# Performance work log

Hardware: AMD Instinct MI355X
Metric: run time of the kernel (lower is better)

## Reference

```python
import jax, jax.numpy as jnp
from jax import lax
import numpy as np

B, T = 256, 512
CHAR_SIZE, CHAR_DIM, HIDDEN = 10000, 50, 256
HALF = HIDDEN // 2  # per-direction hidden size


def _lstm_dir(x, Wih, Whh, bih, bhh, reverse):
    # x: [B,T,D]; Wih: [4H,D]; Whh: [4H,H]; gate order i,f,g,o (PyTorch)
    Bsz = x.shape[0]
    H = Whh.shape[1]
    xg = jnp.einsum('btd,gd->btg', x, Wih) + bih + bhh  # precompute input gates [B,T,4H]
    def step(carry, gt):
        h, c = carry
        g = gt + h @ Whh.T
        i, f, gg, o = jnp.split(g, 4, axis=-1)
        c = jax.nn.sigmoid(f) * c + jax.nn.sigmoid(i) * jnp.tanh(gg)
        h = jax.nn.sigmoid(o) * jnp.tanh(c)
        return (h, c), h
    init = (jnp.zeros((Bsz, H), x.dtype), jnp.zeros((Bsz, H), x.dtype))
    _, hs = lax.scan(step, init, jnp.swapaxes(xg, 0, 1), reverse=reverse)
    return jnp.swapaxes(hs, 0, 1)  # [B,T,H]


def setup_inputs() -> dict:
    key = jax.random.key(0)
    ks = jax.random.split(key, 10)
    scale = np.sqrt(3.0 / CHAR_DIM)
    inp = {
        'user_text_idx': jax.random.randint(ks[0], (B, T), 0, CHAR_SIZE),
        'masks': jnp.ones((B, T), jnp.float32),
        'emb': jax.random.uniform(ks[1], (CHAR_SIZE, CHAR_DIM), jnp.float32, -scale, scale),
        'Wih_f': jax.random.normal(ks[2], (4 * HALF, CHAR_DIM), jnp.float32) * 0.08,
        'Whh_f': jax.random.normal(ks[3], (4 * HALF, HALF), jnp.float32) * 0.08,
        'bih_f': jnp.zeros((4 * HALF,), jnp.float32),
        'bhh_f': jnp.zeros((4 * HALF,), jnp.float32),
        'Wih_b': jax.random.normal(ks[4], (4 * HALF, CHAR_DIM), jnp.float32) * 0.08,
        'Whh_b': jax.random.normal(ks[5], (4 * HALF, HALF), jnp.float32) * 0.08,
        'bih_b': jnp.zeros((4 * HALF,), jnp.float32),
        'bhh_b': jnp.zeros((4 * HALF,), jnp.float32),
    }
    return inp


def reference(user_text_idx, masks, emb, Wih_f, Whh_f, bih_f, bhh_f, Wih_b, Whh_b, bih_b, bhh_b):
    x = emb[user_text_idx]                                  # [B,T,D] embedding lookup
    h_f = _lstm_dir(x, Wih_f, Whh_f, bih_f, bhh_f, False)   # forward direction
    h_b = _lstm_dir(x, Wih_b, Whh_b, bih_b, bhh_b, True)    # backward direction
    out = jnp.concatenate([h_f, h_b], axis=-1)              # [B,T,HIDDEN]
    out = out - (1.0 - masks[..., None]) * 1e8              # mask pad positions
    return jnp.max(out, axis=-2)                            # masked max-pool -> [B,HIDDEN]
```

## Files before the change

kernel.cpp:

```cpp
#include <hip/hip_runtime.h>
#include <hip/hip_fp16.h>


#define TT 512
#define CH 2

typedef _Float16 f16;
typedef _Float16 f16x8 __attribute__((ext_vector_type(8)));
typedef float f32x4 __attribute__((ext_vector_type(4)));
typedef unsigned int u32;
typedef unsigned short u16;

static __device__ __forceinline__ u32 packh2(float lo, float hi) {
    union { struct { f16 x, y; } h; u32 u; } cv;
    cv.h.x = (f16)lo; cv.h.y = (f16)hi;
    return cv.u;
}
static __device__ __forceinline__ u16 f16bits(float v) {
    union { f16 h; u16 u; } cv; cv.h = (f16)v; return cv.u;
}
static __device__ __forceinline__ float fexp(float x) {
    return __builtin_amdgcn_exp2f(x * 1.44269504088896341f);
}
static __device__ __forceinline__ float frcp(float x) {
    return __builtin_amdgcn_rcpf(x);
}
static __device__ __forceinline__ float sigf(float x) {
    return frcp(1.f + fexp(-x));
}
static __device__ __forceinline__ float xor8(float x) {
    union { float f; int i; } c; c.f = x;
#if __has_builtin(__builtin_amdgcn_mov_dpp)
    c.i = __builtin_amdgcn_mov_dpp(c.i, 0x128, 0xF, 0xF, 0);
#elif __has_builtin(__builtin_amdgcn_update_dpp)
    c.i = __builtin_amdgcn_update_dpp(c.i, c.i, 0x128, 0xF, 0xF, 0);
#else
    c.i = __builtin_amdgcn_ds_swizzle(c.i, 0x201F);
#endif
    return c.f;
}
static __device__ __forceinline__ float sel4(f32x4 v, int q) {
    return (q & 2) ? ((q & 1) ? v[3] : v[2]) : ((q & 1) ? v[1] : v[0]);
}

__global__ __attribute__((amdgpu_flat_work_group_size(512, 512),
                          amdgpu_waves_per_eu(2, 2)))
void bilstm_mfma_dpp_kernel(const int* __restrict__ idx,
                            const float* __restrict__ masks,
                            const float* __restrict__ emb,
                            const float* __restrict__ Wih_f, const float* __restrict__ Whh_f,
                            const float* __restrict__ bih_f, const float* __restrict__ bhh_f,
                            const float* __restrict__ Wih_b, const float* __restrict__ Whh_b,
                            const float* __restrict__ bih_b, const float* __restrict__ bhh_b,
                            float* __restrict__ out)
{
    __shared__ __align__(16) unsigned char Hbuf[2][6 * 1024];
    __shared__ u16 idx16[CH * TT];
    __shared__ u32 mbits[TT];

    const int tid  = threadIdx.x;
    const int lane = tid & 63;
    const int wv   = tid >> 6;
    const int l15  = lane & 15;
    const int c4   = lane >> 4;
    const int d    = blockIdx.x & 1;
    const int g    = blockIdx.x >> 1;
    const int b0   = g * CH;
    const int rev  = d;

    const int chain = l15 & 1;
    const int cp    = l15 >> 1;
    const int flag  = cp >> 2;
    const int q     = cp & 3;

    const float* Wih = d ? Wih_b : Wih_f;
    const float* Whh = d ? Whh_b : Whh_f;
    const float* bih = d ? bih_b : bih_f;
    const float* bhh = d ? bhh_b : bhh_f;

    for (int i = tid; i < CH * TT; i += 512) {
        const int m = i >> 9, t = i & 511;
        idx16[i] = (u16)idx[(b0 + m) * TT + t];
    }
    if (tid < TT) {
        u32 mb = 0;
        for (int m = 0; m < CH; ++m)
            mb |= (masks[(b0 + m) * TT + tid] != 0.f ? 1u : 0u) << m;
        mbits[tid] = mb;
    }
    for (int i = tid; i < 2 * 6 * 1024 / 4; i += 512)
        ((u32*)Hbuf)[i] = 0u;

    f16x8 w[6][4];
    f32x4 bias4[4];
#pragma unroll
    for (int gt = 0; gt < 4; ++gt) {
        const int n = (wv + gt * 8) * 16 + l15;
        {
            const int nb_ = (wv + gt * 8) * 16 + c4 * 4;
            const float4 bi = *(const float4*)(bih + nb_);
            const float4 bh = *(const float4*)(bhh + nb_);
            bias4[gt][0] = bi.x + bh.x; bias4[gt][1] = bi.y + bh.y;
            bias4[gt][2] = bi.z + bh.z; bias4[gt][3] = bi.w + bh.w;
        }
#pragma unroll
        for (int jj = 0; jj < 4; ++jj) {
            const float2 e = *(const float2*)(Wih + n * 50 + c4 * 8 + jj * 2);
            w[0][gt][2 * jj]     = (f16)e.x;
            w[0][gt][2 * jj + 1] = (f16)e.y;
        }
#pragma unroll
        for (int j = 0; j < 8; ++j) {
            const int k = 32 + c4 * 8 + j;
            float v = 0.f;
            if (k < 50) v = Wih[n * 50 + k];
            w[1][gt][j] = (f16)v;
        }
#pragma unroll
        for (int kt = 2; kt < 6; ++kt) {
            const int kh = (kt - 2) * 32 + c4 * 8;
            const float4 e0 = *(const float4*)(Whh + n * 128 + kh);
            const float4 e1 = *(const float4*)(Whh + n * 128 + kh + 4);
            w[kt][gt][0] = (f16)e0.x; w[kt][gt][1] = (f16)e0.y;
            w[kt][gt][2] = (f16)e0.z; w[kt][gt][3] = (f16)e0.w;
            w[kt][gt][4] = (f16)e1.x; w[kt][gt][5] = (f16)e1.y;
            w[kt][gt][6] = (f16)e1.z; w[kt][gt][7] = (f16)e1.w;
        }
    }

    __syncthreads();

    if (tid < 400) {
        const int pm = tid / 25, ps = tid % 25;
        const int t0  = rev ? (TT - 1) : 0;
        const int row = idx16[(pm & 1) * TT + t0];
        const float2 e = *(const float2*)(emb + row * 50 + ps * 2);
        const int k0 = 2 * ps;
        const int kt = k0 >> 5, c4k = (k0 >> 3) & 3, j = k0 & 7;
        *(u32*)(&Hbuf[0][(kt << 10) + ((c4k * 16 + pm) << 4) + (j << 1)]) =
            packh2(e.x, e.y);
    }
    __syncthreads();

    float cst0 = 0.f, rm0 = -3e38f;

    const int hd     = wv * 16 + c4 * 4 + q;
    const int k0h    = 64 + hd;
    const int wb_kt  = k0h >> 5;
    const int wb_c4k = (k0h >> 3) & 3;
    const int wb_j   = k0h & 7;
    const int wb_off = (wb_kt << 10) + ((wb_c4k * 16 + chain) << 4) + (wb_j << 1)
                     + flag * 128;

    for (int s = 0; s < TT; ++s) {
        const int cur = s & 1;
        const int t   = rev ? (TT - 1 - s) : s;

        float2 e;
        int pk0 = 0;
        const bool pf = (tid < 400) && (s + 1 < TT);
        const int pm = tid / 25, ps = tid % 25;
        if (pf) {
            const int t1  = rev ? (TT - 2 - s) : (s + 1);
            const int row = idx16[(pm & 1) * TT + t1];
            e = *(const float2*)(emb + row * 50 + ps * 2);
            pk0 = 2 * ps;
        }

        const unsigned char* hb = &Hbuf[cur][0];
        f32x4 ai = bias4[0], af = bias4[1], ag = bias4[2], ao = bias4[3];
#pragma unroll
        for (int kt = 0; kt < 6; ++kt) {
            const f16x8 bf = *(const f16x8*)(hb + (kt << 10) + (lane << 4));
            ai = __builtin_amdgcn_mfma_f32_16x16x32_f16(w[kt][0], bf, ai, 0, 0, 0);
            af = __builtin_amdgcn_mfma_f32_16x16x32_f16(w[kt][1], bf, af, 0, 0, 0);
            ag = __builtin_amdgcn_mfma_f32_16x16x32_f16(w[kt][2], bf, ag, 0, 0, 0);
            ao = __builtin_amdgcn_mfma_f32_16x16x32_f16(w[kt][3], bf, ao, 0, 0, 0);
        }

        const float iv = sel4(ai, q);
        const float fv = sel4(af, q);
        const float gv = sel4(ag, q);
        const float ov = sel4(ao, q);

        const bool fB = (flag != 0);
        const float u = fB ? (gv + gv) : fv;
        const float v = fB ? ov : iv;
        const float su = sigf(u);
        const float sv = sigf(v);
        const float tg_send = 2.f * su - 1.f;
        const float tgx = xor8(tg_send);
        const float svx = xor8(sv);
        const float cc = su * cst0 + sv * tgx;
        cst0 = cc;
        const float ccx = xor8(cc);
        const float cc_use = fB ? ccx : cc;
        const float th = 2.f * sigf(cc_use + cc_use) - 1.f;
        const float so_use = fB ? sv : svx;
        const float hh = so_use * th;

        const float pen = ((mbits[t] >> chain) & 1u) ? 0.f : 1e8f;
        rm0 = fmaxf(rm0, hh - pen);

        unsigned char* nb = &Hbuf[cur ^ 1][0];
        {
            const u16 pk = f16bits(hh);
            *(u16*)(nb + wb_off)      = pk;
            *(u16*)(nb + wb_off + 32) = pk;
            *(u16*)(nb + wb_off + 64) = pk;
            *(u16*)(nb + wb_off + 96) = pk;
        }
        if (pf) {
            const int kt = pk0 >> 5, c4k = (pk0 >> 3) & 3, j = pk0 & 7;
            *(u32*)(nb + (kt << 10) + ((c4k * 16 + pm) << 4) + (j << 1)) =
                packh2(e.x, e.y);
        }
        __syncthreads();
    }

    if (!flag) {
        out[(b0 + chain) * 256 + d * 128 + hd] = rm0;
    }
}

extern "C" void kernel_launch(void* const* d_in, const int* in_sizes, int n_in,
                              void* d_out, int out_size, void* d_ws, size_t ws_size,
                              hipStream_t stream) {
    const int*   idx   = (const int*)d_in[0];
    const float* masks = (const float*)d_in[1];
    const float* emb   = (const float*)d_in[2];
    const float* Wih_f = (const float*)d_in[3];
    const float* Whh_f = (const float*)d_in[4];
    const float* bih_f = (const float*)d_in[5];
    const float* bhh_f = (const float*)d_in[6];
    const float* Wih_b = (const float*)d_in[7];
    const float* Whh_b = (const float*)d_in[8];
    const float* bih_b = (const float*)d_in[9];
    const float* bhh_b = (const float*)d_in[10];
    float* out = (float*)d_out;

    bilstm_mfma_dpp_kernel<<<dim3(256), dim3(512), 0, stream>>>(
        idx, masks, emb,
        Wih_f, Whh_f, bih_f, bhh_f,
        Wih_b, Whh_b, bih_b, bhh_b,
        out);
}
```

Measured before the change: 397.8 us.

## Compact LDS hidden-state buffer and cut per-step shared stores

Replaces the 12 KB pre-swizzled MFMA B-operand buffer with a compact per-chain [2][CH][192] f16 vector. Each lane now reads its B fragment with a broadcast-style 16-byte load, so the layout no longer duplicates rows. Hidden writes go from four u16 stores per lane to one packed u32 store from a quarter of the lanes, using a DPP lane exchange to pair neighbours. Embedding prefetch moves to 50 threads in the last wave. The aim is to shrink LDS write traffic and bank conflicts on the per-step critical path, at the cost of an extra DPP op and a possible read-side broadcast pattern.

```diff
diff --git a/kernel.cpp b/kernel.cpp
--- a/kernel.cpp
+++ b/kernel.cpp
@@ -16,9 +16,6 @@
     cv.h.x = (f16)lo; cv.h.y = (f16)hi;
     return cv.u;
 }
-static __device__ __forceinline__ u16 f16bits(float v) {
-    union { f16 h; u16 u; } cv; cv.h = (f16)v; return cv.u;
-}
 static __device__ __forceinline__ float fexp(float x) {
     return __builtin_amdgcn_exp2f(x * 1.44269504088896341f);
 }
@@ -30,13 +27,12 @@
 }
 static __device__ __forceinline__ float xor8(float x) {
     union { float f; int i; } c; c.f = x;
-#if __has_builtin(__builtin_amdgcn_mov_dpp)
-    c.i = __builtin_amdgcn_mov_dpp(c.i, 0x128, 0xF, 0xF, 0);
-#elif __has_builtin(__builtin_amdgcn_update_dpp)
-    c.i = __builtin_amdgcn_update_dpp(c.i, c.i, 0x128, 0xF, 0xF, 0);
-#else
-    c.i = __builtin_amdgcn_ds_swizzle(c.i, 0x201F);
-#endif
+    c.i = __builtin_amdgcn_mov_dpp(c.i, 0x128, 0xF, 0xF, false);
+    return c.f;
+}
+static __device__ __forceinline__ float xor2(float x) {
+    union { float f; int i; } c; c.f = x;
+    c.i = __builtin_amdgcn_mov_dpp(c.i, 0x4E, 0xF, 0xF, false);
     return c.f;
 }
 static __device__ __forceinline__ float sel4(f32x4 v, int q) {
@@ -45,16 +41,16 @@
 
 __global__ __attribute__((amdgpu_flat_work_group_size(512, 512),
                           amdgpu_waves_per_eu(2, 2)))
-void bilstm_mfma_dpp_kernel(const int* __restrict__ idx,
-                            const float* __restrict__ masks,
-                            const float* __restrict__ emb,
-                            const float* __restrict__ Wih_f, const float* __restrict__ Whh_f,
-                            const float* __restrict__ bih_f, const float* __restrict__ bhh_f,
-                            const float* __restrict__ Wih_b, const float* __restrict__ Whh_b,
-                            const float* __restrict__ bih_b, const float* __restrict__ bhh_b,
-                            float* __restrict__ out)
+void bilstm_compact_kernel(const int* __restrict__ idx,
+                           const float* __restrict__ masks,
+                           const float* __restrict__ emb,
+                           const float* __restrict__ Wih_f, const float* __restrict__ Whh_f,
+                           const float* __restrict__ bih_f, const float* __restrict__ bhh_f,
+                           const float* __restrict__ Wih_b, const float* __restrict__ Whh_b,
+                           const float* __restrict__ bih_b, const float* __restrict__ bhh_b,
+                           float* __restrict__ out)
 {
-    __shared__ __align__(16) unsigned char Hbuf[2][6 * 1024];
+    __shared__ __align__(16) u16 Hc[2][CH][192];
     __shared__ u16 idx16[CH * TT];
     __shared__ u32 mbits[TT];
 
@@ -69,9 +65,8 @@
     const int rev  = d;
 
     const int chain = l15 & 1;
-    const int cp    = l15 >> 1;
-    const int flag  = cp >> 2;
-    const int q     = cp & 3;
+    const int q     = (l15 >> 1) & 3;
+    const int role  = l15 >> 3;
 
     const float* Wih = d ? Wih_b : Wih_f;
     const float* Whh = d ? Whh_b : Whh_f;
@@ -88,8 +83,9 @@
             mb |= (masks[(b0 + m) * TT + tid] != 0.f ? 1u : 0u) << m;
         mbits[tid] = mb;
     }
-    for (int i = tid; i < 2 * 6 * 1024 / 4; i += 512)
-        ((u32*)Hbuf)[i] = 0u;
+    if (tid < 2 * CH * 192 / 2) {
+        ((u32*)Hc)[tid] = 0u;
+    }
 
     f16x8 w[6][4];
     f32x4 bias4[4];
@@ -130,48 +126,43 @@
 
     __syncthreads();
 
-    if (tid < 400) {
-        const int pm = tid / 25, ps = tid % 25;
+    const int  tid7 = tid - 448;
+    const bool xthr = (tid7 >= 0) && (tid7 < 50);
+    const int  xch  = xthr ? (tid7 / 25) : 0;
+    const int  xps  = xthr ? (tid7 % 25) : 0;
+
+    if (xthr) {
         const int t0  = rev ? (TT - 1) : 0;
-        const int row = idx16[(pm & 1) * TT + t0];
-        const float2 e = *(const float2*)(emb + row * 50 + ps * 2);
-        const int k0 = 2 * ps;
-        const int kt = k0 >> 5, c4k = (k0 >> 3) & 3, j = k0 & 7;
-        *(u32*)(&Hbuf[0][(kt << 10) + ((c4k * 16 + pm) << 4) + (j << 1)]) =
+        const int row = idx16[xch * TT + t0];
+        const float2 e = *(const float2*)(emb + row * 50 + xps * 2);
+        *(u32*)((unsigned char*)&Hc[0][0][0] + xch * 384 + xps * 4) =
             packh2(e.x, e.y);
     }
     __syncthreads();
 
-    float cst0 = 0.f, rm0 = -3e38f;
-
-    const int hd     = wv * 16 + c4 * 4 + q;
-    const int k0h    = 64 + hd;
-    const int wb_kt  = k0h >> 5;
-    const int wb_c4k = (k0h >> 3) & 3;
-    const int wb_j   = k0h & 7;
-    const int wb_off = (wb_kt << 10) + ((wb_c4k * 16 + chain) << 4) + (wb_j << 1)
-                     + flag * 128;
+    float cst = 0.f, rm = -3e38f;
+
+    const int hd = wv * 16 + c4 * 4 + q;
+    const bool wbthr = (l15 == 0) | (l15 == 1) | (l15 == 4) | (l15 == 5);
 
     for (int s = 0; s < TT; ++s) {
         const int cur = s & 1;
         const int t   = rev ? (TT - 1 - s) : s;
 
         float2 e;
-        int pk0 = 0;
-        const bool pf = (tid < 400) && (s + 1 < TT);
-        const int pm = tid / 25, ps = tid % 25;
+        const bool pf = xthr && (s + 1 < TT);
         if (pf) {
             const int t1  = rev ? (TT - 2 - s) : (s + 1);
-            const int row = idx16[(pm & 1) * TT + t1];
-            e = *(const float2*)(emb + row * 50 + ps * 2);
-            pk0 = 2 * ps;
-        }
-
-        const unsigned char* hb = &Hbuf[cur][0];
+            const int row = idx16[xch * TT + t1];
+            e = *(const float2*)(emb + row * 50 + xps * 2);
+        }
+
+        const unsigned char* hb =
+            (const unsigned char*)&Hc[cur][0][0] + chain * 384;
         f32x4 ai = bias4[0], af = bias4[1], ag = bias4[2], ao = bias4[3];
 #pragma unroll
         for (int kt = 0; kt < 6; ++kt) {
-            const f16x8 bf = *(const f16x8*)(hb + (kt << 10) + (lane << 4));
+            const f16x8 bf = *(const f16x8*)(hb + kt * 64 + c4 * 16);
             ai = __builtin_amdgcn_mfma_f32_16x16x32_f16(w[kt][0], bf, ai, 0, 0, 0);
             af = __builtin_amdgcn_mfma_f32_16x16x32_f16(w[kt][1], bf, af, 0, 0, 0);
             ag = __builtin_amdgcn_mfma_f32_16x16x32_f16(w[kt][2], bf, ag, 0, 0, 0);
@@ -183,43 +174,38 @@
         const float gv = sel4(ag, q);
         const float ov = sel4(ao, q);
 
-        const bool fB = (flag != 0);
-        const float u = fB ? (gv + gv) : fv;
-        const float v = fB ? ov : iv;
-        const float su = sigf(u);
-        const float sv = sigf(v);
+        const bool rB = (role != 0);
+        const float u_in = rB ? (gv + gv) : fv;
+        const float v_in = rB ? ov : iv;
+        const float su = sigf(u_in);
+        const float sv = sigf(v_in);
         const float tg_send = 2.f * su - 1.f;
         const float tgx = xor8(tg_send);
         const float svx = xor8(sv);
-        const float cc = su * cst0 + sv * tgx;
-        cst0 = cc;
+        const float cc = su * cst + sv * tgx;
+        cst = cc;
         const float ccx = xor8(cc);
-        const float cc_use = fB ? ccx : cc;
+        const float cc_use = rB ? ccx : cc;
         const float th = 2.f * sigf(cc_use + cc_use) - 1.f;
-        const float so_use = fB ? sv : svx;
+        const float so_use = rB ? sv : svx;
         const float hh = so_use * th;
 
         const float pen = ((mbits[t] >> chain) & 1u) ? 0.f : 1e8f;
-        rm0 = fmaxf(rm0, hh - pen);
-
-        unsigned char* nb = &Hbuf[cur ^ 1][0];
-        {
-            const u16 pk = f16bits(hh);
-            *(u16*)(nb + wb_off)      = pk;
-            *(u16*)(nb + wb_off + 32) = pk;
-            *(u16*)(nb + wb_off + 64) = pk;
-            *(u16*)(nb + wb_off + 96) = pk;
+        rm = fmaxf(rm, hh - pen);
+
+        unsigned char* nb = (unsigned char*)&Hc[cur ^ 1][0][0];
+        const float hx2 = xor2(hh);
+        if (wbthr) {
+            *(u32*)(nb + chain * 384 + 128 + hd * 2) = packh2(hh, hx2);
         }
         if (pf) {
-            const int kt = pk0 >> 5, c4k = (pk0 >> 3) & 3, j = pk0 & 7;
-            *(u32*)(nb + (kt << 10) + ((c4k * 16 + pm) << 4) + (j << 1)) =
-                packh2(e.x, e.y);
+            *(u32*)(nb + xch * 384 + xps * 4) = packh2(e.x, e.y);
         }
         __syncthreads();
     }
 
-    if (!flag) {
-        out[(b0 + chain) * 256 + d * 128 + hd] = rm0;
+    if (l15 < 8) {
+        out[(b0 + chain) * 256 + d * 128 + hd] = rm;
     }
 }
 
@@ -239,7 +225,7 @@
     const float* bhh_b = (const float*)d_in[10];
     float* out = (float*)d_out;
 
-    bilstm_mfma_dpp_kernel<<<dim3(256), dim3(512), 0, stream>>>(
+    bilstm_compact_kernel<<<dim3(256), dim3(512), 0, stream>>>(
         idx, masks, emb,
         Wih_f, Whh_f, bih_f, bhh_f,
         Wih_b, Whh_b, bih_b, bhh_b,
```

New measurement: 381.4 us. -4.1%, faster.
